# Kernel optimization log

Measured on AMD Instinct MI355X. Metric: run time of the kernel, lower is better.

The kernel has to match this reference:

```python
import jax, jax.numpy as jnp
import numpy as np

COMMITMENT_COST = 0.25


def setup_inputs() -> dict:
    key = jax.random.key(0)
    k1, k2 = jax.random.split(key)
    inputs = jax.random.normal(k1, (256, 512, 64), dtype=jnp.float32)
    embedding = jax.random.normal(k2, (1024, 64), dtype=jnp.float32) * 4.0
    return {"inputs": inputs, "embedding": embedding}


def reference(inputs, embedding):
    # inputs: [B, T, D], embedding: [K, D]
    input_shape = inputs.shape
    D = embedding.shape[-1]
    flat = inputs.reshape(-1, D)  # [N, D]
    # squared-L2 distances: [N, K]
    distances = (
        jnp.sum(flat * flat, axis=1, keepdims=True)
        + jnp.sum(embedding * embedding, axis=1)[None, :]
        - 2.0 * flat @ embedding.T
    )
    encoding_indices = jnp.argmin(distances, axis=1)  # [N]
    # one-hot @ embedding == gather
    quantized = embedding[encoding_indices].reshape(input_shape)  # [B, T, D]
    # squared-L2 commitment / codebook loss
    e_latent_loss = jnp.sum((jax.lax.stop_gradient(quantized) - inputs) ** 2, axis=-1)
    q_latent_loss = jnp.sum((quantized - jax.lax.stop_gradient(inputs)) ** 2, axis=-1)
    quantization_loss = q_latent_loss + COMMITMENT_COST * e_latent_loss  # [B, T]
    # straight-through estimator
    quantized_sg = inputs + jax.lax.stop_gradient(quantized - inputs)
    encoding_indices = encoding_indices.reshape(input_shape[:-1])  # [B, T]
    return quantized_sg, encoding_indices, quantization_loss
```

## Files before the change

kernel.cpp:

```cpp
#include <hip/hip_runtime.h>
#include <hip/hip_bf16.h>

#define D 64
#define KCODES 1024
#define MARGIN 0.25f
#define OFFSET 2048.0f

typedef __attribute__((ext_vector_type(8))) short bf16x8;
typedef __attribute__((ext_vector_type(4))) float f32x4;

__device__ __forceinline__ unsigned short f2bf(float f) {
    union { __hip_bfloat16 h; unsigned short s; } cv;
    cv.h = __float2bfloat16(f);
    return cv.s;
}
__device__ __forceinline__ float bf2f(unsigned short v) {
    union { unsigned short s; __hip_bfloat16 h; } cv;
    cv.s = v;
    return __bfloat162float(cv.h);
}

__device__ __forceinline__ void stage16(const void* g, void* l) {
    __builtin_amdgcn_global_load_lds(
        (const __attribute__((address_space(1))) void*)g,
        (__attribute__((address_space(3))) void*)l, 16, 0, 0);
}

__global__ __launch_bounds__(256) void prep_kernel(
    const float* __restrict__ emb, float* __restrict__ e2, float* __restrict__ e2b,
    unsigned short* __restrict__ ehi, unsigned short* __restrict__ elo,
    unsigned int* __restrict__ counter) {
    int t = blockIdx.x * 256 + threadIdx.x;
    if (t == 0) *counter = 0u;
    if (t < KCODES) {
        const float4* ep = (const float4*)(emb + (size_t)t * D);
        float s0 = 0.f, s1 = 0.f, s2 = 0.f, s3 = 0.f;
#pragma unroll
        for (int i = 0; i < 16; ++i) {
            float4 v = ep[i];
            s0 = fmaf(v.x, v.x, s0);
            s1 = fmaf(v.y, v.y, s1);
            s2 = fmaf(v.z, v.z, s2);
            s3 = fmaf(v.w, v.w, s3);
        }
        float s = (s0 + s1) + (s2 + s3);
        e2[t] = s;
        e2b[t] = s + OFFSET;
    }
    float v = emb[t];
    unsigned short h = f2bf(v);
    ehi[t] = h;
    elo[t] = f2bf(v - bf2f(h));
}

__global__ __launch_bounds__(256, 4) void vq_mfma_kernel(
    const float* __restrict__ x, const float* __restrict__ emb,
    const float* __restrict__ e2b, const unsigned short* __restrict__ ehi,
    const unsigned short* __restrict__ elo, float* __restrict__ out_q,
    float* __restrict__ out_idx, float* __restrict__ out_loss,
    unsigned int* __restrict__ counter, int* __restrict__ flaglist, int flag_cap) {
    __shared__ float4 lds4[2][1024];
    __shared__ int s_bi[128];
    char* ldsc = (char*)&lds4[0][0];
    const int tid = threadIdx.x;
    const int lane = tid & 63;
    const int wave = __builtin_amdgcn_readfirstlane(tid >> 6);
    const int quad = lane >> 4;
    const int l15 = lane & 15;
    const int rowBase = blockIdx.x * 128 + wave * 32;

    bf16x8 ah[2][2], al[2][2];
#pragma unroll
    for (int rs = 0; rs < 2; ++rs) {
        const float* xr = x + (size_t)(rowBase + rs * 16 + l15) * D;
#pragma unroll
        for (int c = 0; c < 2; ++c) {
            const float4* p = (const float4*)(xr + c * 32 + quad * 8);
            float4 f0 = p[0], f1 = p[1];
            float f[8] = {f0.x, f0.y, f0.z, f0.w, f1.x, f1.y, f1.z, f1.w};
            bf16x8 h, l;
#pragma unroll
            for (int j = 0; j < 8; ++j) {
                float v = -2.0f * f[j];
                unsigned short hu = f2bf(v);
                h[j] = (short)hu;
                l[j] = (short)f2bf(v - bf2f(hu));
            }
            ah[rs][c] = h;
            al[rs][c] = l;
        }
    }

    const unsigned short* gs[4];
#pragma unroll
    for (int i = 0; i < 4; ++i) {
        int li = wave * 256 + i * 64 + lane;
        int h = li >> 9, row = (li >> 3) & 63, sl = li & 7;
        gs[i] = (h ? elo : ehi) + row * 64 + (sl ^ (row & 7)) * 8;
    }
    char* wlds0 = ldsc + wave * 4096;

    const int s7 = l15 & 7;
    const int rdA0 = l15 * 128 + ((quad ^ s7) << 4);
    const int rdB0 = l15 * 128 + (((quad + 4) ^ s7) << 4);

    unsigned int m1[2][4], m2[2][4];
#pragma unroll
    for (int rs = 0; rs < 2; ++rs)
#pragma unroll
        for (int r = 0; r < 4; ++r) { m1[rs][r] = 0xFFFFFFFFu; m2[rs][r] = 0xFFFFFFFFu; }

#pragma unroll
    for (int i = 0; i < 4; ++i) stage16(gs[i], wlds0 + i * 1024);
    float e2v[4];
#pragma unroll
    for (int tg = 0; tg < 4; ++tg) e2v[tg] = e2b[tg * 16 + l15];
    __syncthreads();

#pragma unroll 1
    for (int g = 0; g < 16; ++g) {
        float e2n[4];
        if (g < 15) {
            char* wb = wlds0 + (((g + 1) & 1) << 14);
#pragma unroll
            for (int i = 0; i < 4; ++i)
                stage16(gs[i] + (size_t)(g + 1) * 4096, wb + i * 1024);
#pragma unroll
            for (int tg = 0; tg < 4; ++tg)
                e2n[tg] = e2b[(g + 1) * 64 + tg * 16 + l15];
        }
        __builtin_amdgcn_sched_barrier(0);
        const char* rb = ldsc + ((g & 1) << 14);
#pragma unroll
        for (int tg = 0; tg < 4; ++tg) {
            bf16x8 bh0 = *(const bf16x8*)(rb + rdA0 + tg * 2048);
            bf16x8 bh1 = *(const bf16x8*)(rb + rdB0 + tg * 2048);
            bf16x8 bl0 = *(const bf16x8*)(rb + 8192 + rdA0 + tg * 2048);
            bf16x8 bl1 = *(const bf16x8*)(rb + 8192 + rdB0 + tg * 2048);
            const unsigned tt = (unsigned)(g * 4 + tg);
            const float ev = e2v[tg];
            f32x4 c0 = {ev, ev, ev, ev};
#pragma unroll
            for (int rs = 0; rs < 2; ++rs) {
                f32x4 acc = c0;
                acc = __builtin_amdgcn_mfma_f32_16x16x32_bf16(ah[rs][0], bh0, acc, 0, 0, 0);
                acc = __builtin_amdgcn_mfma_f32_16x16x32_bf16(al[rs][0], bh0, acc, 0, 0, 0);
                acc = __builtin_amdgcn_mfma_f32_16x16x32_bf16(ah[rs][0], bl0, acc, 0, 0, 0);
                acc = __builtin_amdgcn_mfma_f32_16x16x32_bf16(ah[rs][1], bh1, acc, 0, 0, 0);
                acc = __builtin_amdgcn_mfma_f32_16x16x32_bf16(al[rs][1], bh1, acc, 0, 0, 0);
                acc = __builtin_amdgcn_mfma_f32_16x16x32_bf16(ah[rs][1], bl1, acc, 0, 0, 0);
#pragma unroll
                for (int r = 0; r < 4; ++r) {
                    unsigned k = (__float_as_uint(acc[r]) & 0xFFFFFFC0u) | tt;
                    unsigned nm2;
                    asm("v_med3_u32 %0, %1, %2, %3"
                        : "=v"(nm2)
                        : "v"(m1[rs][r]), "v"(m2[rs][r]), "v"(k));
                    m2[rs][r] = nm2;
                    m1[rs][r] = (k < m1[rs][r]) ? k : m1[rs][r];
                }
            }
        }
        if (g < 15) {
#pragma unroll
            for (int tg = 0; tg < 4; ++tg) e2v[tg] = e2n[tg];
        }
        __syncthreads();
    }

#pragma unroll
    for (int rs = 0; rs < 2; ++rs)
#pragma unroll
        for (int r = 0; r < 4; ++r) {
            unsigned v1 = m1[rs][r], v2 = m2[rs][r];
            const unsigned my1 = v1;
#pragma unroll
            for (int mask = 1; mask < 16; mask <<= 1) {
                unsigned o1 = __shfl_xor(v1, mask);
                unsigned o2 = __shfl_xor(v2, mask);
                unsigned hi = v1 > o1 ? v1 : o1;
                unsigned lo2 = v2 < o2 ? v2 : o2;
                v2 = lo2 < hi ? lo2 : hi;
                v1 = v1 < o1 ? v1 : o1;
            }
            unsigned long long bal = __ballot(my1 == v1);
            int winl = __ffsll((bal >> (quad * 16)) & 0xFFFFull) - 1;
            int code = (int)(v1 & 63u) * 16 + winl;
            if (l15 == 0) {
                int lrow = wave * 32 + rs * 16 + quad * 4 + r;
                s_bi[lrow] = code;
                float f1 = __uint_as_float(v1 & 0xFFFFFFC0u);
                float f2 = __uint_as_float(v2 & 0xFFFFFFC0u);
                if (f2 - f1 < MARGIN) {
                    unsigned slot = atomicAdd(counter, 1u);
                    if (slot < (unsigned)flag_cap) flaglist[slot] = blockIdx.x * 128 + lrow;
                }
            }
        }
    __syncthreads();

    if (tid < 128) {
        const int row = blockIdx.x * 128 + tid;
        const int bi = s_bi[tid];
        const float4* qp = (const float4*)(emb + (size_t)bi * D);
        const float4* xp = (const float4*)(x + (size_t)row * D);
        float4* oq = (float4*)(out_q + (size_t)row * D);
        float l0 = 0.f, l1 = 0.f, l2 = 0.f, l3 = 0.f;
#pragma unroll
        for (int i = 0; i < 16; ++i) {
            float4 q = qp[i];
            float4 xv = xp[i];
            float a0 = q.x - xv.x, a1 = q.y - xv.y, a2 = q.z - xv.z, a3 = q.w - xv.w;
            l0 = fmaf(a0, a0, l0);
            l1 = fmaf(a1, a1, l1);
            l2 = fmaf(a2, a2, l2);
            l3 = fmaf(a3, a3, l3);
            float4 o;
            o.x = xv.x + a0;
            o.y = xv.y + a1;
            o.z = xv.z + a2;
            o.w = xv.w + a3;
            oq[i] = o;
        }
        float s = (l0 + l1) + (l2 + l3);
        out_idx[row] = (float)bi;
        out_loss[row] = s + 0.25f * s;
    }
}

__global__ __launch_bounds__(256) void rescore_kernel(
    const float* __restrict__ x, const float* __restrict__ emb,
    const float* __restrict__ e2, float* __restrict__ out_q,
    float* __restrict__ out_idx, float* __restrict__ out_loss,
    const unsigned int* __restrict__ counter, const int* __restrict__ flaglist,
    int flag_cap) {
    __shared__ float s_x[8][64];
    __shared__ int s_rows[8];
    __shared__ float s_wd[8][4];
    __shared__ int s_wi[8][4];
    __shared__ float s_a[4][64];
    unsigned int n = *counter;
    if (n > (unsigned)flag_cap) n = (unsigned)flag_cap;
    const int tid = threadIdx.x;
    const int lane = tid & 63;
    const int wv = tid >> 6;
    for (unsigned int b = blockIdx.x; b * 8u < n; b += gridDim.x) {
        const unsigned base = b * 8u;
        unsigned nbu = n - base;
        if (nbu > 8u) nbu = 8u;
        const int nb = (int)nbu;
        if (tid < 8) s_rows[tid] = flaglist[base + (tid < nb ? tid : 0)];
        __syncthreads();
        if (tid < 128) {
            int r = tid >> 4, q4 = tid & 15;
            ((float4*)&s_x[r][0])[q4] = ((const float4*)(x + (size_t)s_rows[r] * D))[q4];
        }
        __syncthreads();

        float bd_[8];
        int bi_[8];
#pragma unroll
        for (int r = 0; r < 8; ++r) { bd_[r] = 3.4e38f; bi_[r] = 0; }
#pragma unroll 1
        for (int kk = 0; kk < 4; ++kk) {
            const int k = tid + kk * 256;
            const float4* ekp = (const float4*)(emb + (size_t)k * D);
            float d0[8], d1[8], d2[8], d3[8];
#pragma unroll
            for (int r = 0; r < 8; ++r) { d0[r] = 0.f; d1[r] = 0.f; d2[r] = 0.f; d3[r] = 0.f; }
#pragma unroll 1
            for (int i = 0; i < 16; ++i) {
                float4 ev = ekp[i];
#pragma unroll
                for (int r = 0; r < 8; ++r) {
                    float4 xv = ((const float4*)&s_x[r][0])[i];
                    d0[r] = fmaf(xv.x, ev.x, d0[r]);
                    d1[r] = fmaf(xv.y, ev.y, d1[r]);
                    d2[r] = fmaf(xv.z, ev.z, d2[r]);
                    d3[r] = fmaf(xv.w, ev.w, d3[r]);
                }
            }
            float e2k = e2[k];
#pragma unroll
            for (int r = 0; r < 8; ++r) {
                float dist = fmaf(-2.0f, (d0[r] + d1[r]) + (d2[r] + d3[r]), e2k);
                if (dist < bd_[r]) { bd_[r] = dist; bi_[r] = k; }
            }
        }
#pragma unroll
        for (int r = 0; r < 8; ++r) {
            float v = bd_[r];
            int ix = bi_[r];
#pragma unroll
            for (int mask = 1; mask < 64; mask <<= 1) {
                float ov = __shfl_xor(v, mask);
                int oi = __shfl_xor(ix, mask);
                bool tk = (ov < v) || (ov == v && oi < ix);
                v = tk ? ov : v;
                ix = tk ? oi : ix;
            }
            if (lane == 0) { s_wd[r][wv] = v; s_wi[r][wv] = ix; }
        }
        __syncthreads();
        if (tid < 8) {
            float v = s_wd[tid][0];
            int ix = s_wi[tid][0];
#pragma unroll
            for (int w = 1; w < 4; ++w) {
                float ov = s_wd[tid][w];
                int oi = s_wi[tid][w];
                bool tk = (ov < v) || (ov == v && oi < ix);
                v = tk ? ov : v;
                ix = tk ? oi : ix;
            }
            s_wi[tid][0] = ix;
        }
        __syncthreads();
#pragma unroll
        for (int pass = 0; pass < 2; ++pass) {
            const int rloc = pass * 4 + wv;
            const int row = s_rows[rloc];
            const int fbi = s_wi[rloc][0];
            const float xe = s_x[rloc][lane];
            const float a = emb[(size_t)fbi * D + lane] - xe;
            if (rloc < nb) out_q[(size_t)row * D + lane] = xe + a;
            s_a[wv][lane] = a * a;
            __syncthreads();
            if (lane == 0 && rloc < nb) {
                float l0 = 0.f, l1 = 0.f, l2 = 0.f, l3 = 0.f;
                for (int i2 = 0; i2 < 16; ++i2) {
                    l0 += s_a[wv][4 * i2 + 0];
                    l1 += s_a[wv][4 * i2 + 1];
                    l2 += s_a[wv][4 * i2 + 2];
                    l3 += s_a[wv][4 * i2 + 3];
                }
                float s = (l0 + l1) + (l2 + l3);
                out_loss[row] = s + 0.25f * s;
                out_idx[row] = (float)fbi;
            }
            __syncthreads();
        }
    }
}

extern "C" void kernel_launch(void* const* d_in, const int* in_sizes, int n_in,
                              void* d_out, int out_size, void* d_ws, size_t ws_size,
                              hipStream_t stream) {
    const float* x = (const float*)d_in[0];
    const float* emb = (const float*)d_in[1];
    const int nrows = in_sizes[0] / D;

    float* out_q = (float*)d_out;
    float* out_idx = out_q + (size_t)nrows * D;
    float* out_loss = out_idx + nrows;

    char* ws = (char*)d_ws;
    float* e2 = (float*)ws;
    float* e2b = (float*)(ws + 4096);
    unsigned short* ehi = (unsigned short*)(ws + 8192);
    unsigned short* elo = (unsigned short*)(ws + 8192 + 131072);
    unsigned int* counter = (unsigned int*)(ws + 8192 + 262144);
    int* flaglist = (int*)(ws + 8192 + 262144 + 64);
    long long avail = (long long)ws_size - (8192 + 262144 + 64);
    int flag_cap = (int)(avail / 4);
    if (flag_cap > 16384) flag_cap = 16384;
    if (flag_cap < 1024) flag_cap = 1024;

    prep_kernel<<<(KCODES * D) / 256, 256, 0, stream>>>(emb, e2, e2b, ehi, elo, counter);
    vq_mfma_kernel<<<nrows / 128, 256, 0, stream>>>(x, emb, e2b, ehi, elo, out_q,
                                                    out_idx, out_loss, counter,
                                                    flaglist, flag_cap);
    rescore_kernel<<<1024, 256, 0, stream>>>(x, emb, e2, out_q, out_idx, out_loss,
                                             counter, flaglist, flag_cap);
}
```

Baseline: 169.9 us.

## Shrink VQ block to two waves with 32-code LDS stages

Halves the block from 4 waves/128 rows to 2 waves/64 rows and the codebook staging chunk from 64 to 32 codes per iteration, doubling the loop count to 32. The cooperative LDS staging mapping is rewritten for 128 threads and LDS use per block drops to 16KB. This doubles the grid size (2048 blocks) to improve occupancy and tail balance. In exchange, each codebook chunk is reused across fewer rows and there are twice as many barriers per block.

```diff
diff --git a/kernel.cpp b/kernel.cpp
--- a/kernel.cpp
+++ b/kernel.cpp
@@ -53,21 +53,21 @@
     elo[t] = f2bf(v - bf2f(h));
 }
 
-__global__ __launch_bounds__(256, 4) void vq_mfma_kernel(
+__global__ __launch_bounds__(128, 4) void vq_mfma_kernel(
     const float* __restrict__ x, const float* __restrict__ emb,
     const float* __restrict__ e2b, const unsigned short* __restrict__ ehi,
     const unsigned short* __restrict__ elo, float* __restrict__ out_q,
     float* __restrict__ out_idx, float* __restrict__ out_loss,
     unsigned int* __restrict__ counter, int* __restrict__ flaglist, int flag_cap) {
-    __shared__ float4 lds4[2][1024];
-    __shared__ int s_bi[128];
+    __shared__ float4 lds4[2][512];
+    __shared__ int s_bi[64];
     char* ldsc = (char*)&lds4[0][0];
     const int tid = threadIdx.x;
     const int lane = tid & 63;
     const int wave = __builtin_amdgcn_readfirstlane(tid >> 6);
     const int quad = lane >> 4;
     const int l15 = lane & 15;
-    const int rowBase = blockIdx.x * 128 + wave * 32;
+    const int rowBase = blockIdx.x * 64 + wave * 32;
 
     bf16x8 ah[2][2], al[2][2];
 #pragma unroll
@@ -94,11 +94,11 @@
     const unsigned short* gs[4];
 #pragma unroll
     for (int i = 0; i < 4; ++i) {
-        int li = wave * 256 + i * 64 + lane;
-        int h = li >> 9, row = (li >> 3) & 63, sl = li & 7;
+        int li = i * 128 + tid;
+        int h = li >> 8, row = (li >> 3) & 31, sl = li & 7;
         gs[i] = (h ? elo : ehi) + row * 64 + (sl ^ (row & 7)) * 8;
     }
-    char* wlds0 = ldsc + wave * 4096;
+    char* wbase = ldsc + wave * 1024;
 
     const int s7 = l15 & 7;
     const int rdA0 = l15 * 128 + ((quad ^ s7) << 4);
@@ -111,34 +111,32 @@
         for (int r = 0; r < 4; ++r) { m1[rs][r] = 0xFFFFFFFFu; m2[rs][r] = 0xFFFFFFFFu; }
 
 #pragma unroll
-    for (int i = 0; i < 4; ++i) stage16(gs[i], wlds0 + i * 1024);
-    float e2v[4];
-#pragma unroll
-    for (int tg = 0; tg < 4; ++tg) e2v[tg] = e2b[tg * 16 + l15];
+    for (int i = 0; i < 4; ++i) stage16(gs[i], wbase + i * 2048);
+    float e2v0 = e2b[l15];
+    float e2v1 = e2b[16 + l15];
     __syncthreads();
 
 #pragma unroll 1
-    for (int g = 0; g < 16; ++g) {
-        float e2n[4];
-        if (g < 15) {
-            char* wb = wlds0 + (((g + 1) & 1) << 14);
+    for (int g = 0; g < 32; ++g) {
+        float e2n0, e2n1;
+        if (g < 31) {
+            char* wb = wbase + (((g + 1) & 1) << 13);
 #pragma unroll
             for (int i = 0; i < 4; ++i)
-                stage16(gs[i] + (size_t)(g + 1) * 4096, wb + i * 1024);
-#pragma unroll
-            for (int tg = 0; tg < 4; ++tg)
-                e2n[tg] = e2b[(g + 1) * 64 + tg * 16 + l15];
+                stage16(gs[i] + (size_t)(g + 1) * 2048, wb + i * 2048);
+            e2n0 = e2b[(g + 1) * 32 + l15];
+            e2n1 = e2b[(g + 1) * 32 + 16 + l15];
         }
         __builtin_amdgcn_sched_barrier(0);
-        const char* rb = ldsc + ((g & 1) << 14);
-#pragma unroll
-        for (int tg = 0; tg < 4; ++tg) {
-            bf16x8 bh0 = *(const bf16x8*)(rb + rdA0 + tg * 2048);
-            bf16x8 bh1 = *(const bf16x8*)(rb + rdB0 + tg * 2048);
-            bf16x8 bl0 = *(const bf16x8*)(rb + 8192 + rdA0 + tg * 2048);
-            bf16x8 bl1 = *(const bf16x8*)(rb + 8192 + rdB0 + tg * 2048);
-            const unsigned tt = (unsigned)(g * 4 + tg);
-            const float ev = e2v[tg];
+        const char* rb = ldsc + ((g & 1) << 13);
+#pragma unroll
+        for (int tg = 0; tg < 2; ++tg) {
+            bf16x8 bh0 = *(const bf16x8*)(rb + tg * 2048 + rdA0);
+            bf16x8 bh1 = *(const bf16x8*)(rb + tg * 2048 + rdB0);
+            bf16x8 bl0 = *(const bf16x8*)(rb + 4096 + tg * 2048 + rdA0);
+            bf16x8 bl1 = *(const bf16x8*)(rb + 4096 + tg * 2048 + rdB0);
+            const unsigned tt = (unsigned)(g * 2 + tg);
+            const float ev = tg ? e2v1 : e2v0;
             f32x4 c0 = {ev, ev, ev, ev};
 #pragma unroll
             for (int rs = 0; rs < 2; ++rs) {
@@ -161,10 +159,7 @@
                 }
             }
         }
-        if (g < 15) {
-#pragma unroll
-            for (int tg = 0; tg < 4; ++tg) e2v[tg] = e2n[tg];
-        }
+        if (g < 31) { e2v0 = e2n0; e2v1 = e2n1; }
         __syncthreads();
     }
 
@@ -193,14 +188,14 @@
                 float f2 = __uint_as_float(v2 & 0xFFFFFFC0u);
                 if (f2 - f1 < MARGIN) {
                     unsigned slot = atomicAdd(counter, 1u);
-                    if (slot < (unsigned)flag_cap) flaglist[slot] = blockIdx.x * 128 + lrow;
+                    if (slot < (unsigned)flag_cap) flaglist[slot] = blockIdx.x * 64 + lrow;
                 }
             }
         }
     __syncthreads();
 
-    if (tid < 128) {
-        const int row = blockIdx.x * 128 + tid;
+    if (tid < 64) {
+        const int row = blockIdx.x * 64 + tid;
         const int bi = s_bi[tid];
         const float4* qp = (const float4*)(emb + (size_t)bi * D);
         const float4* xp = (const float4*)(x + (size_t)row * D);
@@ -367,9 +362,9 @@
     if (flag_cap < 1024) flag_cap = 1024;
 
     prep_kernel<<<(KCODES * D) / 256, 256, 0, stream>>>(emb, e2, e2b, ehi, elo, counter);
-    vq_mfma_kernel<<<nrows / 128, 256, 0, stream>>>(x, emb, e2b, ehi, elo, out_q,
-                                                    out_idx, out_loss, counter,
-                                                    flaglist, flag_cap);
+    vq_mfma_kernel<<<nrows / 64, 128, 0, stream>>>(x, emb, e2b, ehi, elo, out_q,
+                                                   out_idx, out_loss, counter,
+                                                   flaglist, flag_cap);
     rescore_kernel<<<1024, 256, 0, stream>>>(x, emb, e2, out_q, out_idx, out_loss,
                                              counter, flaglist, flag_cap);
 }
```

After: 171.4 us. About the same (+0.9%).
